# Kernel optimization log

Hardware: AMD Instinct MI355X
Metric: run time of the kernel (lower is better)

## Reference

```python
import jax, jax.numpy as jnp
import numpy as np

EPS = 1e-3    # Keras BatchNormalization default epsilon
ALPHA = 0.3   # Keras LeakyReLU default negative slope


def _bn(x, axes):
    # BatchNormalization(center=False, scale=False) in training mode: batch stats
    m = jnp.mean(x, axis=axes, keepdims=True)
    v = jnp.var(x, axis=axes, keepdims=True)
    return (x - m) * jax.lax.rsqrt(v + EPS)


def _leaky(x):
    return jnp.where(x > 0, x, ALPHA * x)


def setup_inputs() -> dict:
    key = jax.random.key(0)
    ks = jax.random.split(key, 8)
    B, A, D, Hid, H, hd = 8192, 16, 256, 512, 8, 64
    s = 0.02
    return {
        "state": jax.random.normal(ks[0], (B, A, D), jnp.float32),
        "agent_index": 3,
        "Ws": jax.random.normal(ks[1], (D, Hid), jnp.float32) * s,
        "bs": jnp.zeros((Hid,), jnp.float32),
        "Wc": jax.random.normal(ks[2], (D, Hid), jnp.float32) * s,
        "bc": jnp.zeros((Hid,), jnp.float32),
        "Wk": jax.random.normal(ks[3], (H, Hid, hd), jnp.float32) * s,
        "Wq": jax.random.normal(ks[4], (H, Hid, hd), jnp.float32) * s,
        "Wv": jax.random.normal(ks[5], (H, Hid, hd), jnp.float32) * s,
    }


def reference(state, agent_index, Ws, bs, Wc, bc, Wk, Wq, Wv):
    B = state.shape[0]
    H, _, hd = Wk.shape
    ai = int(agent_index)

    # current agent encoder: BN over batch, Dense, LeakyReLU -> [B, Hid]
    cur = state[:, ai, :]
    s_enc = _leaky(_bn(cur, (0,)) @ Ws + bs)

    # other agents encoder: BN over (batch, agent), Dense, LeakyReLU -> [B, A-1, Hid]
    others = jnp.concatenate([state[:, :ai, :], state[:, ai + 1:, :]], axis=1)
    sa_enc = _leaky(_bn(others, (0, 1)) @ Wc + bc)

    # batched per-head projections (replaces the python loop over heads)
    k = jnp.einsum('ban,hnd->bhad', sa_enc, Wk)           # [B,H,A-1,hd]
    v = _leaky(jnp.einsum('ban,hnd->bhad', sa_enc, Wv))   # [B,H,A-1,hd]
    q = jnp.einsum('bn,hnd->bhd', s_enc, Wq)              # [B,H,hd]

    scores = jnp.einsum('bhd,bhad->bha', q, k) / jnp.sqrt(jnp.float32(hd))
    w = jax.nn.softmax(scores, axis=-1)                   # [B,H,A-1]
    att = jnp.einsum('bha,bhad->bhd', w, v)               # [B,H,hd]

    # concat heads in order -> [B, H*hd]
    return att.reshape(B, H * hd)
```

## Files before the change

kernel.cpp:

```cpp
#include <hip/hip_runtime.h>

typedef __attribute__((ext_vector_type(8))) short short8;
typedef __attribute__((ext_vector_type(8))) unsigned short ushort8;
typedef __attribute__((ext_vector_type(4))) unsigned short bfu4;
typedef __attribute__((ext_vector_type(4))) float f32x4;

__device__ __forceinline__ unsigned short f2bf(float f){
  unsigned int u = __builtin_bit_cast(unsigned int, f);
  u += 0x7fffu + ((u >> 16) & 1u);
  return (unsigned short)(u >> 16);
}
__device__ __forceinline__ float bf2f(unsigned short h){
  unsigned int u = ((unsigned int)h) << 16;
  return __builtin_bit_cast(float, u);
}
__device__ __forceinline__ float leaky(float x){ return x > 0.f ? x : 0.3f * x; }

__global__ __launch_bounds__(256) void ca_stats_partial(const float* __restrict__ state,
    const int* __restrict__ agp, float* __restrict__ part, int B){
  int d = threadIdx.x;
  int ag = agp[0];
  int bPer = (B + 255) >> 8;
  int b0 = blockIdx.x * bPer;
  float sC = 0.f, ssC = 0.f, sO = 0.f, ssO = 0.f;
  for (int b = 0; b < bPer; b++){
    int bb = b0 + b;
    if (bb >= B) break;
    const float* row = state + ((size_t)bb << 12);
    #pragma unroll
    for (int a = 0; a < 16; a++){
      float v = row[a*256 + d];
      bool isC = (a == ag);
      sC  += isC ? v   : 0.f;
      ssC += isC ? v*v : 0.f;
      sO  += isC ? 0.f : v;
      ssO += isC ? 0.f : v*v;
    }
  }
  float* p = part + (size_t)blockIdx.x * 1024;
  p[d] = sC; p[d+256] = ssC; p[d+512] = sO; p[d+768] = ssO;
}

__global__ __launch_bounds__(1024) void ca_stats_final(const float* __restrict__ part,
    float* __restrict__ stats, int nblk, int B){
  int d = threadIdx.x & 255, sl = threadIdx.x >> 8;
  float sC = 0.f, ssC = 0.f, sO = 0.f, ssO = 0.f;
  for (int g = sl; g < nblk; g += 4){
    const float* p = part + (size_t)g * 1024;
    sC += p[d]; ssC += p[d+256]; sO += p[d+512]; ssO += p[d+768];
  }
  __shared__ float red[4][4][256];
  red[sl][0][d] = sC; red[sl][1][d] = ssC; red[sl][2][d] = sO; red[sl][3][d] = ssO;
  __syncthreads();
  if (sl == 0){
    sC  = red[0][0][d] + red[1][0][d] + red[2][0][d] + red[3][0][d];
    ssC = red[0][1][d] + red[1][1][d] + red[2][1][d] + red[3][1][d];
    sO  = red[0][2][d] + red[1][2][d] + red[2][2][d] + red[3][2][d];
    ssO = red[0][3][d] + red[1][3][d] + red[2][3][d] + red[3][3][d];
    float nC = (float)B, nO = (float)B * 15.f;
    float mC = sC / nC, vC = ssC / nC - mC * mC;
    float mO = sO / nO, vO = ssO / nO - mO * mO;
    float rC = rsqrtf(vC + 1e-3f), rO = rsqrtf(vO + 1e-3f);
    stats[d] = rC; stats[d+256] = mC * rC; stats[d+512] = rO; stats[d+768] = mO * rO;
  }
}

__global__ __launch_bounds__(256) void ca_prep_sc(const float* __restrict__ Ws,
    const float* __restrict__ bs, const float* __restrict__ Wc, const float* __restrict__ bc,
    const float* __restrict__ stats, unsigned short* __restrict__ WsT,
    unsigned short* __restrict__ WcT, unsigned short* __restrict__ WsF,
    unsigned short* __restrict__ WcF, float* __restrict__ bsp, float* __restrict__ bcp){
  int n = blockIdx.x, d = threadIdx.x;
  float rC = stats[d], mrC = stats[d+256], rO = stats[d+512], mrO = stats[d+768];
  float ws = Ws[(size_t)d*512 + n], wc = Wc[(size_t)d*512 + n];
  unsigned short wsb = f2bf(ws * rC), wcb = f2bf(wc * rO);
  WsT[(size_t)n*256 + d] = wsb;
  WcT[(size_t)n*256 + d] = wcb;
  {
    int h = n >> 6, nt = (n >> 4) & 3, j = n & 15;
    int kk = d >> 5, hi = (d >> 3) & 3, e = d & 7;
    size_t fi = (size_t)((h*8 + kk)*4 + nt)*512 + (hi*16 + j)*8 + e;
    WsF[fi] = wsb;
    WcF[fi] = wcb;
  }
  __shared__ float red[256];
  red[d] = mrC * ws;
  __syncthreads();
  for (int s = 128; s > 0; s >>= 1){ if (d < s) red[d] += red[d+s]; __syncthreads(); }
  if (d == 0) bsp[n] = bs[n] - red[0];
  __syncthreads();
  red[d] = mrO * wc;
  __syncthreads();
  for (int s = 128; s > 0; s >>= 1){ if (d < s) red[d] += red[d+s]; __syncthreads(); }
  if (d == 0) bcp[n] = bc[n] - red[0];
}

__global__ __launch_bounds__(512) void ca_prep_kvq(const float* __restrict__ Wk,
    const float* __restrict__ Wv, const float* __restrict__ Wq,
    unsigned short* __restrict__ WkT, unsigned short* __restrict__ WvT,
    unsigned short* __restrict__ WqT, unsigned short* __restrict__ WkF2,
    unsigned short* __restrict__ WvF, unsigned short* __restrict__ WqF){
  int c = blockIdx.x & 511, m = blockIdx.x >> 9;
  int n = threadIdx.x;
  if (m == 3){
    size_t idx = (size_t)c*512 + n;
    int h = (int)(idx >> 15), nn = (int)((idx >> 6) & 511), dd = (int)(idx & 63);
    int nt = nn >> 4, j = nn & 15, kq = dd >> 5, hi = (dd >> 3) & 3, e = dd & 7;
    WkF2[(size_t)((h*32 + nt)*2 + kq)*512 + (hi*16 + j)*8 + e] = f2bf(Wk[idx]);
    return;
  }
  int h = c >> 6, dd = c & 63;
  const float* W = (m == 0) ? Wk : (m == 1) ? Wv : Wq;
  unsigned short* O = (m == 0) ? WkT : (m == 1) ? WvT : WqT;
  float scale = (m == 2) ? 0.125f : 1.f;
  unsigned short v = f2bf(W[((size_t)h*512 + n)*64 + dd] * scale);
  O[(size_t)c*512 + n] = v;
  if (m != 0){
    int nt = (c >> 4) & 3, j = c & 15;
    int kk = n >> 5, hi = (n >> 3) & 3, e = n & 7;
    size_t fi = (size_t)((h*16 + kk)*4 + nt)*512 + (hi*16 + j)*8 + e;
    if (m == 1) WvF[fi] = v; else WqF[fi] = v;
  }
}

__global__ __launch_bounds__(512) void ca_q_kernel(const float* __restrict__ state,
    const int* __restrict__ agp,
    const unsigned short* __restrict__ WsT, const float* __restrict__ bsp,
    const unsigned short* __restrict__ WqT, unsigned short* __restrict__ Qws){
  __shared__ unsigned short U[32*512];
  __shared__ float bias_s[512];
  unsigned short* Alds = U;
  unsigned short* SE = U;
  int tid = threadIdx.x, lane = tid & 63, w = tid >> 6;
  int j = lane & 15, hi = lane >> 4;
  int b0 = blockIdx.x * 32;
  int ag = agp[0];

  for (int s = tid; s < 32*32; s += 512){
    int row = s >> 5, kg = s & 31;
    const float* p = state + (((size_t)(b0 + row) * 16 + ag) << 8) + kg * 8;
    f32x4 v0 = *(const f32x4*)p, v1 = *(const f32x4*)(p + 4);
    ushort8 hv;
    hv[0]=f2bf(v0[0]); hv[1]=f2bf(v0[1]); hv[2]=f2bf(v0[2]); hv[3]=f2bf(v0[3]);
    hv[4]=f2bf(v1[0]); hv[5]=f2bf(v1[1]); hv[6]=f2bf(v1[2]); hv[7]=f2bf(v1[3]);
    *(ushort8*)&Alds[row*256 + ((kg ^ (row & 7)) << 3)] = hv;
  }
  bias_s[tid & 511] = bsp[tid & 511];
  __syncthreads();

  int cb = w * 64;
  f32x4 zero4 = {0.f, 0.f, 0.f, 0.f};
  f32x4 acc[2][4];
  #pragma unroll
  for (int a1 = 0; a1 < 2; a1++)
    #pragma unroll
    for (int a2 = 0; a2 < 4; a2++) acc[a1][a2] = zero4;

  #pragma unroll
  for (int kk = 0; kk < 8; kk++){
    short8 bfr[4];
    #pragma unroll
    for (int nt = 0; nt < 4; nt++)
      bfr[nt] = *(const short8*)&WsT[(size_t)(cb + nt*16 + j)*256 + kk*32 + hi*8];
    #pragma unroll
    for (int mt = 0; mt < 2; mt++){
      int row = mt*16 + j;
      short8 afr = *(const short8*)&Alds[row*256 + ((((kk << 2) | hi) ^ (row & 7)) << 3)];
      #pragma unroll
      for (int nt = 0; nt < 4; nt++)
        acc[mt][nt] = __builtin_amdgcn_mfma_f32_16x16x32_bf16(afr, bfr[nt], acc[mt][nt], 0, 0, 0);
    }
  }
  __syncthreads();
  #pragma unroll
  for (int mt = 0; mt < 2; mt++)
    #pragma unroll
    for (int nt = 0; nt < 4; nt++)
      #pragma unroll
      for (int i = 0; i < 4; i++){
        int row = mt*16 + hi*4 + i, col = cb + nt*16 + j;
        float x = leaky(acc[mt][nt][i] + bias_s[col]);
        SE[row*512 + ((((col >> 3) ^ (row & 7)) << 3) | (col & 7))] = f2bf(x);
      }
  __syncthreads();

  f32x4 qa[2][4];
  #pragma unroll
  for (int a1 = 0; a1 < 2; a1++)
    #pragma unroll
    for (int a2 = 0; a2 < 4; a2++) qa[a1][a2] = zero4;
  #pragma unroll
  for (int kk = 0; kk < 16; kk++){
    short8 bfr[4];
    #pragma unroll
    for (int nt = 0; nt < 4; nt++)
      bfr[nt] = *(const short8*)&WqT[(size_t)(cb + nt*16 + j)*512 + kk*32 + hi*8];
    #pragma unroll
    for (int mt = 0; mt < 2; mt++){
      int row = mt*16 + j;
      short8 afr = *(const short8*)&SE[row*512 + ((((kk << 2) | hi) ^ (row & 7)) << 3)];
      #pragma unroll
      for (int nt = 0; nt < 4; nt++)
        qa[mt][nt] = __builtin_amdgcn_mfma_f32_16x16x32_bf16(afr, bfr[nt], qa[mt][nt], 0, 0, 0);
    }
  }
  #pragma unroll
  for (int mt = 0; mt < 2; mt++)
    #pragma unroll
    for (int nt = 0; nt < 4; nt++)
      #pragma unroll
      for (int i = 0; i < 4; i++)
        Qws[(size_t)(b0 + mt*16 + hi*4 + i)*512 + cb + nt*16 + j] = f2bf(qa[mt][nt][i]);
}

__global__ __launch_bounds__(512) void ca_q_kernel_qk(const float* __restrict__ state,
    const int* __restrict__ agp,
    const unsigned short* __restrict__ WsF, const float* __restrict__ bsp,
    const unsigned short* __restrict__ WqF, const unsigned short* __restrict__ WkF2,
    unsigned short* __restrict__ QKws){
  __shared__ unsigned short U[32*512];
  __shared__ float bias_s[512];
  unsigned short* Alds = U;
  unsigned short* SE = U;
  unsigned short* Qlds = U;
  int tid = threadIdx.x, lane = tid & 63, w = tid >> 6;
  int j = lane & 15, hi = lane >> 4;
  int b0 = blockIdx.x * 32;
  int ag = agp[0];

  for (int s = tid; s < 32*32; s += 512){
    int row = s >> 5, kg = s & 31;
    const float* p = state + (((size_t)(b0 + row) * 16 + ag) << 8) + kg * 8;
    f32x4 v0 = *(const f32x4*)p, v1 = *(const f32x4*)(p + 4);
    ushort8 hv;
    hv[0]=f2bf(v0[0]); hv[1]=f2bf(v0[1]); hv[2]=f2bf(v0[2]); hv[3]=f2bf(v0[3]);
    hv[4]=f2bf(v1[0]); hv[5]=f2bf(v1[1]); hv[6]=f2bf(v1[2]); hv[7]=f2bf(v1[3]);
    *(ushort8*)&Alds[row*256 + ((kg ^ (row & 7)) << 3)] = hv;
  }
  bias_s[tid & 511] = bsp[tid & 511];
  __syncthreads();

  int cb = w * 64;
  f32x4 zero4 = {0.f, 0.f, 0.f, 0.f};
  f32x4 acc[2][4];
  #pragma unroll
  for (int a1 = 0; a1 < 2; a1++)
    #pragma unroll
    for (int a2 = 0; a2 < 4; a2++) acc[a1][a2] = zero4;

  #pragma unroll
  for (int kk = 0; kk < 8; kk++){
    short8 bfr[4];
    #pragma unroll
    for (int nt = 0; nt < 4; nt++)
      bfr[nt] = *(const short8*)&WsF[(size_t)((w*8 + kk)*4 + nt)*512 + lane*8];
    #pragma unroll
    for (int mt = 0; mt < 2; mt++){
      int row = mt*16 + j;
      short8 afr = *(const short8*)&Alds[row*256 + ((((kk << 2) | hi) ^ (row & 7)) << 3)];
      #pragma unroll
      for (int nt = 0; nt < 4; nt++)
        acc[mt][nt] = __builtin_amdgcn_mfma_f32_16x16x32_bf16(afr, bfr[nt], acc[mt][nt], 0, 0, 0);
    }
  }
  __syncthreads();
  #pragma unroll
  for (int mt = 0; mt < 2; mt++)
    #pragma unroll
    for (int nt = 0; nt < 4; nt++)
      #pragma unroll
      for (int i = 0; i < 4; i++){
        int row = mt*16 + hi*4 + i, col = cb + nt*16 + j;
        float x = leaky(acc[mt][nt][i] + bias_s[col]);
        SE[row*512 + ((((col >> 3) ^ (row & 7)) << 3) | (col & 7))] = f2bf(x);
      }
  __syncthreads();

  f32x4 qa[2][4];
  #pragma unroll
  for (int a1 = 0; a1 < 2; a1++)
    #pragma unroll
    for (int a2 = 0; a2 < 4; a2++) qa[a1][a2] = zero4;
  #pragma unroll
  for (int kk = 0; kk < 16; kk++){
    short8 bfr[4];
    #pragma unroll
    for (int nt = 0; nt < 4; nt++)
      bfr[nt] = *(const short8*)&WqF[(size_t)((w*16 + kk)*4 + nt)*512 + lane*8];
    #pragma unroll
    for (int mt = 0; mt < 2; mt++){
      int row = mt*16 + j;
      short8 afr = *(const short8*)&SE[row*512 + ((((kk << 2) | hi) ^ (row & 7)) << 3)];
      #pragma unroll
      for (int nt = 0; nt < 4; nt++)
        qa[mt][nt] = __builtin_amdgcn_mfma_f32_16x16x32_bf16(afr, bfr[nt], qa[mt][nt], 0, 0, 0);
    }
  }
  __syncthreads();
  #pragma unroll
  for (int mt = 0; mt < 2; mt++)
    #pragma unroll
    for (int nt = 0; nt < 4; nt++)
      #pragma unroll
      for (int i = 0; i < 4; i++){
        int row = mt*16 + hi*4 + i, col = cb + nt*16 + j;
        Qlds[row*512 + ((((col >> 3) ^ (row & 7)) << 3) | (col & 7))] = f2bf(qa[mt][nt][i]);
      }
  __syncthreads();

  short8 aq[2][2];
  #pragma unroll
  for (int bt = 0; bt < 2; bt++)
    #pragma unroll
    for (int kq = 0; kq < 2; kq++){
      int row = bt*16 + j;
      int col = w*64 + kq*32 + hi*8;
      aq[bt][kq] = *(const short8*)&Qlds[row*512 + ((((col >> 3) ^ (row & 7)) << 3))];
    }
  for (int nt = 0; nt < 32; nt++){
    short8 bf0 = *(const short8*)&WkF2[(size_t)((w*32 + nt)*2 + 0)*512 + lane*8];
    short8 bf1 = *(const short8*)&WkF2[(size_t)((w*32 + nt)*2 + 1)*512 + lane*8];
    #pragma unroll
    for (int bt = 0; bt < 2; bt++){
      f32x4 qt = zero4;
      qt = __builtin_amdgcn_mfma_f32_16x16x32_bf16(bf0, aq[bt][0], qt, 0, 0, 0);
      qt = __builtin_amdgcn_mfma_f32_16x16x32_bf16(bf1, aq[bt][1], qt, 0, 0, 0);
      bfu4 pk;
      pk[0] = f2bf(qt[0]); pk[1] = f2bf(qt[1]); pk[2] = f2bf(qt[2]); pk[3] = f2bf(qt[3]);
      *(bfu4*)&QKws[((size_t)(b0 + bt*16 + j)*8 + w)*512 + nt*16 + hi*4] = pk;
    }
  }
}

__global__ __launch_bounds__(512) void ca_main_kernel_qk(const float* __restrict__ state,
    const int* __restrict__ agp,
    const unsigned short* __restrict__ WcF, const float* __restrict__ bcp,
    const unsigned short* __restrict__ WvF, const unsigned short* __restrict__ QKws,
    float* __restrict__ out){
  __shared__ unsigned short U[128*512];
  __shared__ float bias_s[512];
  __shared__ float Wl[8*16*8];
  unsigned short* Alds = U;
  unsigned short* SA = U;
  int tid = threadIdx.x, lane = tid & 63, w = tid >> 6;
  int j = lane & 15, hi = lane >> 4;
  int b0 = blockIdx.x * 8;
  int ag = agp[0];
  f32x4 zero4 = {0.f, 0.f, 0.f, 0.f};
  short8 zero8 = {0,0,0,0,0,0,0,0};

  #pragma unroll
  for (int g = 0; g < 2; g++){
    f32x4 st0[4], st1[4];
    #pragma unroll
    for (int it = 0; it < 4; it++){
      int s = tid + 512*(g*4 + it);
      int row = s >> 5, kg = s & 31;
      int bl = row >> 4, ai = row & 15;
      if (ai < 15){
        int a = ai + (ai >= ag ? 1 : 0);
        const float* p = state + (((size_t)(b0 + bl) * 16 + a) << 8) + kg * 8;
        st0[it] = *(const f32x4*)p;
        st1[it] = *(const f32x4*)(p + 4);
      } else { st0[it] = zero4; st1[it] = zero4; }
    }
    #pragma unroll
    for (int it = 0; it < 4; it++){
      int s = tid + 512*(g*4 + it);
      int row = s >> 5, kg = s & 31;
      ushort8 hv;
      hv[0]=f2bf(st0[it][0]); hv[1]=f2bf(st0[it][1]); hv[2]=f2bf(st0[it][2]); hv[3]=f2bf(st0[it][3]);
      hv[4]=f2bf(st1[it][0]); hv[5]=f2bf(st1[it][1]); hv[6]=f2bf(st1[it][2]); hv[7]=f2bf(st1[it][3]);
      *(ushort8*)&Alds[row*256 + ((kg ^ (row & 7)) << 3)] = hv;
    }
  }
  bias_s[tid] = bcp[tid];
  __syncthreads();

  int cb = w * 64;

  f32x4 acc[8][4];
  #pragma unroll
  for (int a1 = 0; a1 < 8; a1++)
    #pragma unroll
    for (int a2 = 0; a2 < 4; a2++) acc[a1][a2] = zero4;
  {
    short8 bcur[4], bnxt[4];
    #pragma unroll
    for (int nt = 0; nt < 4; nt++)
      bcur[nt] = *(const short8*)&WcF[(size_t)((w*8 + 0)*4 + nt)*512 + lane*8];
    #pragma unroll 1
    for (int kk = 0; kk < 8; kk++){
      if (kk < 7){
        #pragma unroll
        for (int nt = 0; nt < 4; nt++)
          bnxt[nt] = *(const short8*)&WcF[(size_t)((w*8 + kk + 1)*4 + nt)*512 + lane*8];
      }
      #pragma unroll
      for (int mt = 0; mt < 8; mt++){
        int row = mt*16 + j;
        short8 afr = *(const short8*)&Alds[row*256 + ((((kk << 2) | hi) ^ (row & 7)) << 3)];
        #pragma unroll
        for (int nt = 0; nt < 4; nt++)
          acc[mt][nt] = __builtin_amdgcn_mfma_f32_16x16x32_bf16(afr, bcur[nt], acc[mt][nt], 0, 0, 0);
      }
      #pragma unroll
      for (int nt = 0; nt < 4; nt++) bcur[nt] = bnxt[nt];
    }
  }
  __syncthreads();
  #pragma unroll
  for (int mt = 0; mt < 8; mt++)
    #pragma unroll
    for (int nt = 0; nt < 4; nt++)
      #pragma unroll
      for (int i = 0; i < 4; i++){
        int row = mt*16 + hi*4 + i, col = cb + nt*16 + j;
        float x = leaky(acc[mt][nt][i] + bias_s[col]);
        SA[row*512 + ((((col >> 3) ^ (row & 7)) << 3) | (col & 7))] = f2bf(x);
      }
  __syncthreads();

  f32x4 qs = zero4;
  {
    size_t qbase = ((size_t)(b0 + w)*8 + (j & 7))*512;
    #pragma unroll
    for (int kk = 0; kk < 16; kk++){
      short8 bq = *(const short8*)&QKws[qbase + kk*32 + hi*8];
      if (j >= 8) bq = zero8;
      int row = w*16 + j;
      short8 afr = *(const short8*)&SA[row*512 + ((((kk << 2) | hi) ^ (row & 7)) << 3)];
      qs = __builtin_amdgcn_mfma_f32_16x16x32_bf16(afr, bq, qs, 0, 0, 0);
    }
  }
  {
    float sv0 = qs[0], sv1 = qs[1], sv2 = qs[2], sv3 = qs[3];
    sv3 = (hi == 3) ? -1e30f : sv3;
    float m = fmaxf(fmaxf(sv0, sv1), fmaxf(sv2, sv3));
    m = fmaxf(m, __shfl_xor(m, 16)); m = fmaxf(m, __shfl_xor(m, 32));
    float e0 = __expf(sv0-m), e1 = __expf(sv1-m), e2 = __expf(sv2-m), e3 = __expf(sv3-m);
    float sum = e0 + e1 + e2 + e3;
    sum += __shfl_xor(sum, 16); sum += __shfl_xor(sum, 32);
    float inv = 1.f / sum;
    if (j < 8){
      Wl[w*128 + (hi*4+0)*8 + j] = e0*inv;
      Wl[w*128 + (hi*4+1)*8 + j] = e1*inv;
      Wl[w*128 + (hi*4+2)*8 + j] = e2*inv;
      Wl[w*128 + (hi*4+3)*8 + j] = e3*inv;
    }
  }

  f32x4 va[8][4];
  #pragma unroll
  for (int a1 = 0; a1 < 8; a1++)
    #pragma unroll
    for (int a2 = 0; a2 < 4; a2++) va[a1][a2] = zero4;
  {
    short8 bcur[4], bnxt[4];
    #pragma unroll
    for (int nt = 0; nt < 4; nt++)
      bcur[nt] = *(const short8*)&WvF[(size_t)((w*16 + 0)*4 + nt)*512 + lane*8];
    #pragma unroll 1
    for (int kk = 0; kk < 16; kk++){
      if (kk < 15){
        #pragma unroll
        for (int nt = 0; nt < 4; nt++)
          bnxt[nt] = *(const short8*)&WvF[(size_t)((w*16 + kk + 1)*4 + nt)*512 + lane*8];
      }
      #pragma unroll
      for (int mt = 0; mt < 8; mt++){
        int row = mt*16 + j;
        short8 afr = *(const short8*)&SA[row*512 + ((((kk << 2) | hi) ^ (row & 7)) << 3)];
        #pragma unroll
        for (int nt = 0; nt < 4; nt++)
          va[mt][nt] = __builtin_amdgcn_mfma_f32_16x16x32_bf16(afr, bcur[nt], va[mt][nt], 0, 0, 0);
      }
      #pragma unroll
      for (int nt = 0; nt < 4; nt++) bcur[nt] = bnxt[nt];
    }
  }
  __syncthreads();

  #pragma unroll
  for (int mt = 0; mt < 8; mt++){
    float w0 = Wl[mt*128 + (hi*4+0)*8 + w];
    float w1 = Wl[mt*128 + (hi*4+1)*8 + w];
    float w2 = Wl[mt*128 + (hi*4+2)*8 + w];
    float w3 = Wl[mt*128 + (hi*4+3)*8 + w];
    float ap0 = w0*leaky(va[mt][0][0]) + w1*leaky(va[mt][0][1]) + w2*leaky(va[mt][0][2]) + w3*leaky(va[mt][0][3]);
    float ap1 = w0*leaky(va[mt][1][0]) + w1*leaky(va[mt][1][1]) + w2*leaky(va[mt][1][2]) + w3*leaky(va[mt][1][3]);
    float ap2 = w0*leaky(va[mt][2][0]) + w1*leaky(va[mt][2][1]) + w2*leaky(va[mt][2][2]) + w3*leaky(va[mt][2][3]);
    float ap3 = w0*leaky(va[mt][3][0]) + w1*leaky(va[mt][3][1]) + w2*leaky(va[mt][3][2]) + w3*leaky(va[mt][3][3]);
    ap0 += __shfl_xor(ap0, 16); ap0 += __shfl_xor(ap0, 32);
    ap1 += __shfl_xor(ap1, 16); ap1 += __shfl_xor(ap1, 32);
    ap2 += __shfl_xor(ap2, 16); ap2 += __shfl_xor(ap2, 32);
    ap3 += __shfl_xor(ap3, 16); ap3 += __shfl_xor(ap3, 32);
    float val = (hi == 0) ? ap0 : (hi == 1) ? ap1 : (hi == 2) ? ap2 : ap3;
    out[(size_t)(b0 + mt)*512 + cb + lane] = val;
  }
}

__global__ __launch_bounds__(512) void ca_main_kernel(const float* __restrict__ state,
    const int* __restrict__ agp,
    const unsigned short* __restrict__ WcT, const float* __restrict__ bcp,
    const unsigned short* __restrict__ WkT, const unsigned short* __restrict__ WvT,
    const unsigned short* __restrict__ Qws, float* __restrict__ out){
  __shared__ unsigned short U[128*512];
  __shared__ unsigned short Qs[8*512];
  __shared__ float bias_s[512];
  unsigned short* Alds = U;
  unsigned short* SA = U;
  int tid = threadIdx.x, lane = tid & 63, w = tid >> 6;
  int j = lane & 15, hi = lane >> 4;
  int b0 = blockIdx.x * 8;
  int ag = agp[0];
  f32x4 zero4 = {0.f, 0.f, 0.f, 0.f};

  #pragma unroll
  for (int g = 0; g < 2; g++){
    f32x4 st0[4], st1[4];
    #pragma unroll
    for (int it = 0; it < 4; it++){
      int s = tid + 512*(g*4 + it);
      int row = s >> 5, kg = s & 31;
      int bl = row >> 4, ai = row & 15;
      if (ai < 15){
        int a = ai + (ai >= ag ? 1 : 0);
        const float* p = state + (((size_t)(b0 + bl) * 16 + a) << 8) + kg * 8;
        st0[it] = *(const f32x4*)p;
        st1[it] = *(const f32x4*)(p + 4);
      } else { st0[it] = zero4; st1[it] = zero4; }
    }
    #pragma unroll
    for (int it = 0; it < 4; it++){
      int s = tid + 512*(g*4 + it);
      int row = s >> 5, kg = s & 31;
      ushort8 hv;
      hv[0]=f2bf(st0[it][0]); hv[1]=f2bf(st0[it][1]); hv[2]=f2bf(st0[it][2]); hv[3]=f2bf(st0[it][3]);
      hv[4]=f2bf(st1[it][0]); hv[5]=f2bf(st1[it][1]); hv[6]=f2bf(st1[it][2]); hv[7]=f2bf(st1[it][3]);
      *(ushort8*)&Alds[row*256 + ((kg ^ (row & 7)) << 3)] = hv;
    }
  }
  *(ushort8*)&Qs[tid*8] = *(const ushort8*)&Qws[(size_t)b0*512 + tid*8];
  bias_s[tid] = bcp[tid];
  __syncthreads();

  int cb = w * 64;

  f32x4 acc[8][4];
  #pragma unroll
  for (int a1 = 0; a1 < 8; a1++)
    #pragma unroll
    for (int a2 = 0; a2 < 4; a2++) acc[a1][a2] = zero4;
  {
    short8 bcur[4], bnxt[4];
    #pragma unroll
    for (int nt = 0; nt < 4; nt++)
      bcur[nt] = *(const short8*)&WcT[(size_t)(cb + nt*16 + j)*256 + hi*8];
    #pragma unroll 1
    for (int kk = 0; kk < 8; kk++){
      if (kk < 7){
        #pragma unroll
        for (int nt = 0; nt < 4; nt++)
          bnxt[nt] = *(const short8*)&WcT[(size_t)(cb + nt*16 + j)*256 + (kk+1)*32 + hi*8];
      }
      #pragma unroll
      for (int mt = 0; mt < 8; mt++){
        int row = mt*16 + j;
        short8 afr = *(const short8*)&Alds[row*256 + ((((kk << 2) | hi) ^ (row & 7)) << 3)];
        #pragma unroll
        for (int nt = 0; nt < 4; nt++)
          acc[mt][nt] = __builtin_amdgcn_mfma_f32_16x16x32_bf16(afr, bcur[nt], acc[mt][nt], 0, 0, 0);
      }
      #pragma unroll
      for (int nt = 0; nt < 4; nt++) bcur[nt] = bnxt[nt];
    }
  }
  __syncthreads();
  #pragma unroll
  for (int mt = 0; mt < 8; mt++)
    #pragma unroll
    for (int nt = 0; nt < 4; nt++)
      #pragma unroll
      for (int i = 0; i < 4; i++){
        int row = mt*16 + hi*4 + i, col = cb + nt*16 + j;
        float x = leaky(acc[mt][nt][i] + bias_s[col]);
        SA[row*512 + ((((col >> 3) ^ (row & 7)) << 3) | (col & 7))] = f2bf(x);
      }
  __syncthreads();

  f32x4 ka[8][4];
  #pragma unroll
  for (int a1 = 0; a1 < 8; a1++)
    #pragma unroll
    for (int a2 = 0; a2 < 4; a2++) ka[a1][a2] = zero4;
  {
    short8 bcur[4], bnxt[4];
    #pragma unroll
    for (int nt = 0; nt < 4; nt++)
      bcur[nt] = *(const short8*)&WkT[(size_t)(cb + nt*16 + j)*512 + hi*8];
    #pragma unroll 1
    for (int kk = 0; kk < 16; kk++){
      if (kk < 15){
        #pragma unroll
        for (int nt = 0; nt < 4; nt++)
          bnxt[nt] = *(const short8*)&WkT[(size_t)(cb + nt*16 + j)*512 + (kk+1)*32 + hi*8];
      }
      #pragma unroll
      for (int mt = 0; mt < 8; mt++){
        int row = mt*16 + j;
        short8 afr = *(const short8*)&SA[row*512 + ((((kk << 2) | hi) ^ (row & 7)) << 3)];
        #pragma unroll
        for (int nt = 0; nt < 4; nt++)
          ka[mt][nt] = __builtin_amdgcn_mfma_f32_16x16x32_bf16(afr, bcur[nt], ka[mt][nt], 0, 0, 0);
      }
      #pragma unroll
      for (int nt = 0; nt < 4; nt++) bcur[nt] = bnxt[nt];
    }
  }

  float wgt[8][4];
  #pragma unroll
  for (int mt = 0; mt < 8; mt++){
    float sv[4];
    #pragma unroll
    for (int i = 0; i < 4; i++){
      float t = 0.f;
      #pragma unroll
      for (int nt = 0; nt < 4; nt++)
        t += bf2f(Qs[mt*512 + cb + nt*16 + j]) * ka[mt][nt][i];
      t += __shfl_xor(t, 1); t += __shfl_xor(t, 2);
      t += __shfl_xor(t, 4); t += __shfl_xor(t, 8);
      sv[i] = t;
    }
    sv[3] = (hi == 3) ? -1e30f : sv[3];
    float m = fmaxf(fmaxf(sv[0], sv[1]), fmaxf(sv[2], sv[3]));
    m = fmaxf(m, __shfl_xor(m, 16)); m = fmaxf(m, __shfl_xor(m, 32));
    float e0 = __expf(sv[0]-m), e1 = __expf(sv[1]-m), e2 = __expf(sv[2]-m), e3 = __expf(sv[3]-m);
    float sum = e0 + e1 + e2 + e3;
    sum += __shfl_xor(sum, 16); sum += __shfl_xor(sum, 32);
    float inv = 1.f / sum;
    wgt[mt][0] = e0*inv; wgt[mt][1] = e1*inv; wgt[mt][2] = e2*inv; wgt[mt][3] = e3*inv;
  }

  f32x4 va[8][4];
  #pragma unroll
  for (int a1 = 0; a1 < 8; a1++)
    #pragma unroll
    for (int a2 = 0; a2 < 4; a2++) va[a1][a2] = zero4;
  {
    short8 bcur[4], bnxt[4];
    #pragma unroll
    for (int nt = 0; nt < 4; nt++)
      bcur[nt] = *(const short8*)&WvT[(size_t)(cb + nt*16 + j)*512 + hi*8];
    #pragma unroll 1
    for (int kk = 0; kk < 16; kk++){
      if (kk < 15){
        #pragma unroll
        for (int nt = 0; nt < 4; nt++)
          bnxt[nt] = *(const short8*)&WvT[(size_t)(cb + nt*16 + j)*512 + (kk+1)*32 + hi*8];
      }
      #pragma unroll
      for (int mt = 0; mt < 8; mt++){
        int row = mt*16 + j;
        short8 afr = *(const short8*)&SA[row*512 + ((((kk << 2) | hi) ^ (row & 7)) << 3)];
        #pragma unroll
        for (int nt = 0; nt < 4; nt++)
          va[mt][nt] = __builtin_amdgcn_mfma_f32_16x16x32_bf16(afr, bcur[nt], va[mt][nt], 0, 0, 0);
      }
      #pragma unroll
      for (int nt = 0; nt < 4; nt++) bcur[nt] = bnxt[nt];
    }
  }

  #pragma unroll
  for (int mt = 0; mt < 8; mt++){
    float ap0 = 0.f, ap1 = 0.f, ap2 = 0.f, ap3 = 0.f;
    #pragma unroll
    for (int i = 0; i < 4; i++){
      float wv = wgt[mt][i];
      ap0 += wv * leaky(va[mt][0][i]);
      ap1 += wv * leaky(va[mt][1][i]);
      ap2 += wv * leaky(va[mt][2][i]);
      ap3 += wv * leaky(va[mt][3][i]);
    }
    ap0 += __shfl_xor(ap0, 16); ap0 += __shfl_xor(ap0, 32);
    ap1 += __shfl_xor(ap1, 16); ap1 += __shfl_xor(ap1, 32);
    ap2 += __shfl_xor(ap2, 16); ap2 += __shfl_xor(ap2, 32);
    ap3 += __shfl_xor(ap3, 16); ap3 += __shfl_xor(ap3, 32);
    float val = (hi == 0) ? ap0 : (hi == 1) ? ap1 : (hi == 2) ? ap2 : ap3;
    out[(size_t)(b0 + mt)*512 + cb + lane] = val;
  }
}

extern "C" void kernel_launch(void* const* d_in, const int* in_sizes, int n_in,
                              void* d_out, int out_size, void* d_ws, size_t ws_size,
                              hipStream_t stream) {
  const float* state = (const float*)d_in[0];
  const int*   agp   = (const int*)d_in[1];
  const float* Ws    = (const float*)d_in[2];
  const float* bs    = (const float*)d_in[3];
  const float* Wc    = (const float*)d_in[4];
  const float* bc    = (const float*)d_in[5];
  const float* Wk    = (const float*)d_in[6];
  const float* Wq    = (const float*)d_in[7];
  const float* Wv    = (const float*)d_in[8];
  float* out = (float*)d_out;
  int B = in_sizes[0] / 4096;

  char* wsb = (char*)d_ws;
  float* part  = (float*)wsb;
  float* stats = (float*)(wsb + (1 << 20));
  float* bsp   = (float*)(wsb + (1 << 20) + 4096);
  float* bcp   = (float*)(wsb + (1 << 20) + 6144);
  unsigned short* WsT  = (unsigned short*)(wsb + (1 << 20) + 8192);
  unsigned short* WcT  = WsT  + 512*256;
  unsigned short* WkT  = WcT  + 512*256;
  unsigned short* WvT  = WkT  + 512*512;
  unsigned short* WqT  = WvT  + 512*512;
  unsigned short* WkF2 = WqT  + 512*512;
  unsigned short* Qws  = WkF2 + 512*512;
  unsigned short* QKws = Qws  + (size_t)B*512;
  unsigned short* WsF  = Qws;
  unsigned short* WcF  = WsF + 512*256;
  unsigned short* WqF  = WcF + 512*256;
  unsigned short* WvF  = WqF + 512*512;

  size_t need = ((size_t)(1 << 20) + 8192)
              + 2ull*(512*256 + 512*256 + 512*512 + 512*512 + 512*512 + 512*512)
              + 2ull*B*512 + 2ull*B*8*512;
  bool qkp = (ws_size >= need);

  hipLaunchKernelGGL(ca_stats_partial, dim3(256), dim3(256), 0, stream, state, agp, part, B);
  hipLaunchKernelGGL(ca_stats_final,   dim3(1),   dim3(1024), 0, stream, part, stats, 256, B);
  hipLaunchKernelGGL(ca_prep_sc,       dim3(512), dim3(256), 0, stream, Ws, bs, Wc, bc, stats, WsT, WcT, WsF, WcF, bsp, bcp);
  hipLaunchKernelGGL(ca_prep_kvq,      dim3(2048),dim3(512), 0, stream, Wk, Wv, Wq, WkT, WvT, WqT, WkF2, WvF, WqF);
  if (qkp){
    hipLaunchKernelGGL(ca_q_kernel_qk,   dim3(B/32),dim3(512), 0, stream, state, agp, WsF, bsp, WqF, WkF2, QKws);
    hipLaunchKernelGGL(ca_main_kernel_qk,dim3(B/8), dim3(512), 0, stream, state, agp, WcF, bcp, WvF, QKws, out);
  } else {
    hipLaunchKernelGGL(ca_q_kernel,      dim3(B/32),dim3(512), 0, stream, state, agp, WsT, bsp, WqT, Qws);
    hipLaunchKernelGGL(ca_main_kernel,   dim3(B/8), dim3(512), 0, stream, state, agp, WcT, bcp, WkT, WvT, Qws, out);
  }
}
```

Before: 236.7 us.

## Use padded LDS rows with transposed MFMA writeback, split stats across more threads

Replaces the XOR-swizzled LDS layout for the encoder activations with a padded row stride (520), and swaps the MFMA operand order so each lane holds 4 consecutive columns and can write them as one packed 8-byte store instead of scalar stores. The Q/QK kernel now processes 16 rows per block instead of 32, doubling the grid, and the stats-partial kernel uses 1024 threads with an LDS reduction. The goal is fewer LDS store instructions, cheaper addressing and more parallelism in the small kernels. The padded layout may bring back bank conflicts on reads, and the larger shared array in the main kernel may lower occupancy.

```diff
diff --git a/kernel.cpp b/kernel.cpp
--- a/kernel.cpp
+++ b/kernel.cpp
@@ -16,16 +16,18 @@
 }
 __device__ __forceinline__ float leaky(float x){ return x > 0.f ? x : 0.3f * x; }
 
-__global__ __launch_bounds__(256) void ca_stats_partial(const float* __restrict__ state,
+#define SAS 520
+
+__global__ __launch_bounds__(1024) void ca_stats_partial(const float* __restrict__ state,
     const int* __restrict__ agp, float* __restrict__ part, int B){
-  int d = threadIdx.x;
+  int d = threadIdx.x & 255, sl = threadIdx.x >> 8;
   int ag = agp[0];
   int bPer = (B + 255) >> 8;
   int b0 = blockIdx.x * bPer;
   float sC = 0.f, ssC = 0.f, sO = 0.f, ssO = 0.f;
-  for (int b = 0; b < bPer; b++){
+  for (int b = sl; b < bPer; b += 4){
     int bb = b0 + b;
-    if (bb >= B) break;
+    if (bb >= B) continue;
     const float* row = state + ((size_t)bb << 12);
     #pragma unroll
     for (int a = 0; a < 16; a++){
@@ -37,8 +39,16 @@
       ssO += isC ? 0.f : v*v;
     }
   }
-  float* p = part + (size_t)blockIdx.x * 1024;
-  p[d] = sC; p[d+256] = ssC; p[d+512] = sO; p[d+768] = ssO;
+  __shared__ float red[4][4][256];
+  red[sl][0][d] = sC; red[sl][1][d] = ssC; red[sl][2][d] = sO; red[sl][3][d] = ssO;
+  __syncthreads();
+  if (sl == 0){
+    float* p = part + (size_t)blockIdx.x * 1024;
+    p[d]     = red[0][0][d] + red[1][0][d] + red[2][0][d] + red[3][0][d];
+    p[d+256] = red[0][1][d] + red[1][1][d] + red[2][1][d] + red[3][1][d];
+    p[d+512] = red[0][2][d] + red[1][2][d] + red[2][2][d] + red[3][2][d];
+    p[d+768] = red[0][3][d] + red[1][3][d] + red[2][3][d] + red[3][3][d];
+  }
 }
 
 __global__ __launch_bounds__(1024) void ca_stats_final(const float* __restrict__ part,
@@ -218,18 +228,19 @@
     const unsigned short* __restrict__ WsF, const float* __restrict__ bsp,
     const unsigned short* __restrict__ WqF, const unsigned short* __restrict__ WkF2,
     unsigned short* __restrict__ QKws){
-  __shared__ unsigned short U[32*512];
+  __shared__ unsigned short U[16*SAS];
   __shared__ float bias_s[512];
   unsigned short* Alds = U;
   unsigned short* SE = U;
   unsigned short* Qlds = U;
   int tid = threadIdx.x, lane = tid & 63, w = tid >> 6;
   int j = lane & 15, hi = lane >> 4;
-  int b0 = blockIdx.x * 32;
+  int b0 = blockIdx.x * 16;
   int ag = agp[0];
-
-  for (int s = tid; s < 32*32; s += 512){
-    int row = s >> 5, kg = s & 31;
+  f32x4 zero4 = {0.f, 0.f, 0.f, 0.f};
+
+  {
+    int row = tid >> 5, kg = tid & 31;
     const float* p = state + (((size_t)(b0 + row) * 16 + ag) << 8) + kg * 8;
     f32x4 v0 = *(const f32x4*)p, v1 = *(const f32x4*)(p + 4);
     ushort8 hv;
@@ -237,98 +248,74 @@
     hv[4]=f2bf(v1[0]); hv[5]=f2bf(v1[1]); hv[6]=f2bf(v1[2]); hv[7]=f2bf(v1[3]);
     *(ushort8*)&Alds[row*256 + ((kg ^ (row & 7)) << 3)] = hv;
   }
-  bias_s[tid & 511] = bsp[tid & 511];
+  bias_s[tid] = bsp[tid];
   __syncthreads();
 
   int cb = w * 64;
-  f32x4 zero4 = {0.f, 0.f, 0.f, 0.f};
-  f32x4 acc[2][4];
-  #pragma unroll
-  for (int a1 = 0; a1 < 2; a1++)
-    #pragma unroll
-    for (int a2 = 0; a2 < 4; a2++) acc[a1][a2] = zero4;
-
+
+  f32x4 acc[4];
+  #pragma unroll
+  for (int a2 = 0; a2 < 4; a2++) acc[a2] = zero4;
   #pragma unroll
   for (int kk = 0; kk < 8; kk++){
     short8 bfr[4];
     #pragma unroll
     for (int nt = 0; nt < 4; nt++)
       bfr[nt] = *(const short8*)&WsF[(size_t)((w*8 + kk)*4 + nt)*512 + lane*8];
-    #pragma unroll
-    for (int mt = 0; mt < 2; mt++){
-      int row = mt*16 + j;
-      short8 afr = *(const short8*)&Alds[row*256 + ((((kk << 2) | hi) ^ (row & 7)) << 3)];
-      #pragma unroll
-      for (int nt = 0; nt < 4; nt++)
-        acc[mt][nt] = __builtin_amdgcn_mfma_f32_16x16x32_bf16(afr, bfr[nt], acc[mt][nt], 0, 0, 0);
-    }
-  }
-  __syncthreads();
-  #pragma unroll
-  for (int mt = 0; mt < 2; mt++)
-    #pragma unroll
-    for (int nt = 0; nt < 4; nt++)
-      #pragma unroll
-      for (int i = 0; i < 4; i++){
-        int row = mt*16 + hi*4 + i, col = cb + nt*16 + j;
-        float x = leaky(acc[mt][nt][i] + bias_s[col]);
-        SE[row*512 + ((((col >> 3) ^ (row & 7)) << 3) | (col & 7))] = f2bf(x);
-      }
-  __syncthreads();
-
-  f32x4 qa[2][4];
-  #pragma unroll
-  for (int a1 = 0; a1 < 2; a1++)
-    #pragma unroll
-    for (int a2 = 0; a2 < 4; a2++) qa[a1][a2] = zero4;
+    short8 afr = *(const short8*)&Alds[j*256 + ((((kk << 2) | hi) ^ (j & 7)) << 3)];
+    #pragma unroll
+    for (int nt = 0; nt < 4; nt++)
+      acc[nt] = __builtin_amdgcn_mfma_f32_16x16x32_bf16(bfr[nt], afr, acc[nt], 0, 0, 0);
+  }
+  __syncthreads();
+  #pragma unroll
+  for (int nt = 0; nt < 4; nt++){
+    int nb = cb + nt*16 + hi*4;
+    bfu4 pk;
+    #pragma unroll
+    for (int i = 0; i < 4; i++) pk[i] = f2bf(leaky(acc[nt][i] + bias_s[nb + i]));
+    *(bfu4*)&SE[j*SAS + nb] = pk;
+  }
+  __syncthreads();
+
+  f32x4 qa[4];
+  #pragma unroll
+  for (int a2 = 0; a2 < 4; a2++) qa[a2] = zero4;
   #pragma unroll
   for (int kk = 0; kk < 16; kk++){
     short8 bfr[4];
     #pragma unroll
     for (int nt = 0; nt < 4; nt++)
       bfr[nt] = *(const short8*)&WqF[(size_t)((w*16 + kk)*4 + nt)*512 + lane*8];
-    #pragma unroll
-    for (int mt = 0; mt < 2; mt++){
-      int row = mt*16 + j;
-      short8 afr = *(const short8*)&SE[row*512 + ((((kk << 2) | hi) ^ (row & 7)) << 3)];
-      #pragma unroll
-      for (int nt = 0; nt < 4; nt++)
-        qa[mt][nt] = __builtin_amdgcn_mfma_f32_16x16x32_bf16(afr, bfr[nt], qa[mt][nt], 0, 0, 0);
-    }
-  }
-  __syncthreads();
-  #pragma unroll
-  for (int mt = 0; mt < 2; mt++)
-    #pragma unroll
-    for (int nt = 0; nt < 4; nt++)
-      #pragma unroll
-      for (int i = 0; i < 4; i++){
-        int row = mt*16 + hi*4 + i, col = cb + nt*16 + j;
-        Qlds[row*512 + ((((col >> 3) ^ (row & 7)) << 3) | (col & 7))] = f2bf(qa[mt][nt][i]);
-      }
-  __syncthreads();
-
-  short8 aq[2][2];
-  #pragma unroll
-  for (int bt = 0; bt < 2; bt++)
-    #pragma unroll
-    for (int kq = 0; kq < 2; kq++){
-      int row = bt*16 + j;
-      int col = w*64 + kq*32 + hi*8;
-      aq[bt][kq] = *(const short8*)&Qlds[row*512 + ((((col >> 3) ^ (row & 7)) << 3))];
-    }
+    short8 afr = *(const short8*)&SE[j*SAS + kk*32 + hi*8];
+    #pragma unroll
+    for (int nt = 0; nt < 4; nt++)
+      qa[nt] = __builtin_amdgcn_mfma_f32_16x16x32_bf16(bfr[nt], afr, qa[nt], 0, 0, 0);
+  }
+  __syncthreads();
+  #pragma unroll
+  for (int nt = 0; nt < 4; nt++){
+    int nb = cb + nt*16 + hi*4;
+    bfu4 pk;
+    #pragma unroll
+    for (int i = 0; i < 4; i++) pk[i] = f2bf(qa[nt][i]);
+    *(bfu4*)&Qlds[j*SAS + nb] = pk;
+  }
+  __syncthreads();
+
+  short8 aq[2];
+  #pragma unroll
+  for (int kq = 0; kq < 2; kq++)
+    aq[kq] = *(const short8*)&Qlds[j*SAS + w*64 + kq*32 + hi*8];
   for (int nt = 0; nt < 32; nt++){
     short8 bf0 = *(const short8*)&WkF2[(size_t)((w*32 + nt)*2 + 0)*512 + lane*8];
     short8 bf1 = *(const short8*)&WkF2[(size_t)((w*32 + nt)*2 + 1)*512 + lane*8];
-    #pragma unroll
-    for (int bt = 0; bt < 2; bt++){
-      f32x4 qt = zero4;
-      qt = __builtin_amdgcn_mfma_f32_16x16x32_bf16(bf0, aq[bt][0], qt, 0, 0, 0);
-      qt = __builtin_amdgcn_mfma_f32_16x16x32_bf16(bf1, aq[bt][1], qt, 0, 0, 0);
-      bfu4 pk;
-      pk[0] = f2bf(qt[0]); pk[1] = f2bf(qt[1]); pk[2] = f2bf(qt[2]); pk[3] = f2bf(qt[3]);
-      *(bfu4*)&QKws[((size_t)(b0 + bt*16 + j)*8 + w)*512 + nt*16 + hi*4] = pk;
-    }
+    f32x4 qt = zero4;
+    qt = __builtin_amdgcn_mfma_f32_16x16x32_bf16(bf0, aq[0], qt, 0, 0, 0);
+    qt = __builtin_amdgcn_mfma_f32_16x16x32_bf16(bf1, aq[1], qt, 0, 0, 0);
+    bfu4 pk;
+    pk[0] = f2bf(qt[0]); pk[1] = f2bf(qt[1]); pk[2] = f2bf(qt[2]); pk[3] = f2bf(qt[3]);
+    *(bfu4*)&QKws[((size_t)(b0 + j)*8 + w)*512 + nt*16 + hi*4] = pk;
   }
 }
 
@@ -337,7 +324,7 @@
     const unsigned short* __restrict__ WcF, const float* __restrict__ bcp,
     const unsigned short* __restrict__ WvF, const unsigned short* __restrict__ QKws,
     float* __restrict__ out){
-  __shared__ unsigned short U[128*512];
+  __shared__ unsigned short U[128*SAS];
   __shared__ float bias_s[512];
   __shared__ float Wl[8*16*8];
   unsigned short* Alds = U;
@@ -402,7 +389,7 @@
         short8 afr = *(const short8*)&Alds[row*256 + ((((kk << 2) | hi) ^ (row & 7)) << 3)];
         #pragma unroll
         for (int nt = 0; nt < 4; nt++)
-          acc[mt][nt] = __builtin_amdgcn_mfma_f32_16x16x32_bf16(afr, bcur[nt], acc[mt][nt], 0, 0, 0);
+          acc[mt][nt] = __builtin_amdgcn_mfma_f32_16x16x32_bf16(bcur[nt], afr, acc[mt][nt], 0, 0, 0);
       }
       #pragma unroll
       for (int nt = 0; nt < 4; nt++) bcur[nt] = bnxt[nt];
@@ -412,13 +399,14 @@
   #pragma unroll
   for (int mt = 0; mt < 8; mt++)
     #pragma unroll
-    for (int nt = 0; nt < 4; nt++)
-      #pragma unroll
-      for (int i = 0; i < 4; i++){
-        int row = mt*16 + hi*4 + i, col = cb + nt*16 + j;
-        float x = leaky(acc[mt][nt][i] + bias_s[col]);
-        SA[row*512 + ((((col >> 3) ^ (row & 7)) << 3) | (col & 7))] = f2bf(x);
-      }
+    for (int nt = 0; nt < 4; nt++){
+      int m = mt*16 + j;
+      int nb = cb + nt*16 + hi*4;
+      bfu4 pk;
+      #pragma unroll
+      for (int i = 0; i < 4; i++) pk[i] = f2bf(leaky(acc[mt][nt][i] + bias_s[nb + i]));
+      *(bfu4*)&SA[m*SAS + nb] = pk;
+    }
   __syncthreads();
 
   f32x4 qs = zero4;
@@ -428,8 +416,7 @@
     for (int kk = 0; kk < 16; kk++){
       short8 bq = *(const short8*)&QKws[qbase + kk*32 + hi*8];
       if (j >= 8) bq = zero8;
-      int row = w*16 + j;
-      short8 afr = *(const short8*)&SA[row*512 + ((((kk << 2) | hi) ^ (row & 7)) << 3)];
+      short8 afr = *(const short8*)&SA[(w*16 + j)*SAS + kk*32 + hi*8];
       qs = __builtin_amdgcn_mfma_f32_16x16x32_bf16(afr, bq, qs, 0, 0, 0);
     }
   }
@@ -469,8 +456,7 @@
       }
       #pragma unroll
       for (int mt = 0; mt < 8; mt++){
-        int row = mt*16 + j;
-        short8 afr = *(const short8*)&SA[row*512 + ((((kk << 2) | hi) ^ (row & 7)) << 3)];
+        short8 afr = *(const short8*)&SA[(mt*16 + j)*SAS + kk*32 + hi*8];
         #pragma unroll
         for (int nt = 0; nt < 4; nt++)
           va[mt][nt] = __builtin_amdgcn_mfma_f32_16x16x32_bf16(afr, bcur[nt], va[mt][nt], 0, 0, 0);
@@ -731,12 +717,12 @@
               + 2ull*B*512 + 2ull*B*8*512;
   bool qkp = (ws_size >= need);
 
-  hipLaunchKernelGGL(ca_stats_partial, dim3(256), dim3(256), 0, stream, state, agp, part, B);
+  hipLaunchKernelGGL(ca_stats_partial, dim3(256), dim3(1024), 0, stream, state, agp, part, B);
   hipLaunchKernelGGL(ca_stats_final,   dim3(1),   dim3(1024), 0, stream, part, stats, 256, B);
   hipLaunchKernelGGL(ca_prep_sc,       dim3(512), dim3(256), 0, stream, Ws, bs, Wc, bc, stats, WsT, WcT, WsF, WcF, bsp, bcp);
   hipLaunchKernelGGL(ca_prep_kvq,      dim3(2048),dim3(512), 0, stream, Wk, Wv, Wq, WkT, WvT, WqT, WkF2, WvF, WqF);
   if (qkp){
-    hipLaunchKernelGGL(ca_q_kernel_qk,   dim3(B/32),dim3(512), 0, stream, state, agp, WsF, bsp, WqF, WkF2, QKws);
+    hipLaunchKernelGGL(ca_q_kernel_qk,   dim3(B/16),dim3(512), 0, stream, state, agp, WsF, bsp, WqF, WkF2, QKws);
     hipLaunchKernelGGL(ca_main_kernel_qk,dim3(B/8), dim3(512), 0, stream, state, agp, WcF, bcp, WvF, QKws, out);
   } else {
     hipLaunchKernelGGL(ca_q_kernel,      dim3(B/32),dim3(512), 0, stream, state, agp, WsT, bsp, WqT, Qws);
```

Result: no change. 234.6 us (-0.9%).
